# Kernel optimization log

Hardware: AMD Instinct MI355X
Metric: run time of the kernel (lower is better)

## Reference

```python
import jax, jax.numpy as jnp
import numpy as np

B, N, DX, DZ = 4, 2048, 2, 128
PPD = (128, 128)
GRID_RANGE = ((-2.0, 2.0), (-2.0, 2.0))
INIT_LS = 0.1


def _construct_grid():
    axes = [jnp.linspace(lo, hi, p, dtype=jnp.float32) for (lo, hi), p in zip(GRID_RANGE, PPD)]
    mesh = jnp.meshgrid(*axes, indexing="ij")
    return jnp.stack(mesh, axis=-1)  # [128, 128, 2]


def setup_inputs() -> dict:
    key = jax.random.key(0)
    k1, k2 = jax.random.split(key)
    x = jax.random.uniform(k1, (B, N, DX), dtype=jnp.float32, minval=-2.0, maxval=2.0)
    z = jax.random.normal(k2, (B, N, DZ), dtype=jnp.float32)
    grid = _construct_grid()
    # inverse-softplus of init lengthscale, per dim
    ls0 = jnp.full((DX,), INIT_LS, dtype=jnp.float32)
    lengthscale_param = jnp.log(jnp.exp(ls0) - 1.0)
    return {"x": x, "z": z, "grid": grid, "lengthscale_param": lengthscale_param}


def reference(x, z, grid, lengthscale_param):
    b = x.shape[0]
    grid_shape = grid.shape[:-1]  # (128, 128)
    lengthscale = 1e-05 + jax.nn.softplus(lengthscale_param)  # [dx]
    grid_flat = grid.reshape(-1, grid.shape[-1])  # [M, dx], M = 16384
    # per-dim squared distance / l^2, summed over dx  -> [b, M, n]
    diff = grid_flat[None, :, None, :] - x[:, None, :, :]  # [b, M, n, dx]
    pre_exp = jnp.sum((diff * diff) / (lengthscale ** 2), axis=-1)
    weights = jnp.exp(-0.5 * pre_exp)  # [b, M, n]
    z_grid_flat = jnp.einsum("bmn,bnd->bmd", weights, z)  # [b, M, dz]
    z_grid = z_grid_flat.reshape((b,) + grid_shape + (z.shape[-1],))
    x_grid = jnp.broadcast_to(grid[None], (b,) + grid.shape)
    return (x_grid, z_grid)
```

## Files before the change

### kernel.cpp

```cpp
#include <hip/hip_runtime.h>

#define BATCH 4
#define NPTS  2048
#define DZDIM 128
#define GD    128
#define M_TOT (GD*GD)
#define TN    32
#define PZ    40
#define ZP    2112
#define WBIN  15

typedef __attribute__((ext_vector_type(8))) __bf16 bf16x8;
typedef __attribute__((ext_vector_type(4))) float floatx4;

__device__ __forceinline__ unsigned int f2bf_bits(float x){
  unsigned int u = __float_as_uint(x);
  u += 0x7FFFu + ((u >> 16) & 1u);
  return u >> 16;
}
__device__ __forceinline__ int point_bin(float px){
  int bin = __float2int_rn((px + 2.0f) * (127.0f / 4.0f));
  return min(GD - 1, max(0, bin));
}

__global__ __launch_bounds__(256) void prep_kernel(
    const float* __restrict__ x, const float* __restrict__ grid,
    float* __restrict__ out, int* __restrict__ binStart,
    float2* __restrict__ xs, int* __restrict__ perm)
{
  const int tid = threadIdx.x;
  if (blockIdx.x < BATCH){
    __shared__ int h[GD];
    __shared__ int s[GD + 1];
    const int b = blockIdx.x;
    const float2* __restrict__ x2 = (const float2*)x;
    if (tid < GD) h[tid] = 0;
    __syncthreads();
    float2 xv[8]; int bn[8];
#pragma unroll
    for (int u = 0; u < 8; ++u){
      xv[u] = x2[b*NPTS + u*256 + tid];
      bn[u] = point_bin(xv[u].x);
      atomicAdd(&h[bn[u]], 1);
    }
    __syncthreads();
    if (tid == 0){
      int acc = 0;
#pragma unroll
      for (int j = 0; j < GD; ++j){ s[j] = acc; acc += h[j]; }
      s[GD] = acc;
    }
    __syncthreads();
    if (tid <= GD) binStart[b*(GD+1) + tid] = s[tid];
    if (tid < GD) h[tid] = 0;
    __syncthreads();
#pragma unroll
    for (int u = 0; u < 8; ++u){
      int j = s[bn[u]] + atomicAdd(&h[bn[u]], 1);
      xs[(long)b*ZP + j]       = xv[u];
      perm[b*NPTS + j]         = u*256 + tid;
    }
  } else {
    int idx = (blockIdx.x - BATCH) * 256 + tid;
    float g = grid[idx];
#pragma unroll
    for (int bb = 0; bb < BATCH; ++bb) out[bb*(GD*GD*2) + idx] = g;
  }
}

__global__ __launch_bounds__(256) void ztwy_kernel(
    const float* __restrict__ z, const float2* __restrict__ xs,
    const int* __restrict__ perm, const float* __restrict__ lsp,
    unsigned short* __restrict__ zt, float* __restrict__ wy)
{
  const int b   = blockIdx.y;
  const int jj  = threadIdx.x & 31;
  const int oct = threadIdx.x >> 5;
  if (blockIdx.x >= NPTS/32){
    int j = NPTS + (blockIdx.x - NPTS/32)*32 + jj;
#pragma unroll
    for (int yy = 0; yy < 16; ++yy)
      wy[(long)(b*GD + oct*16 + yy)*ZP + j] = 0.f;
    return;
  }
  const int j = blockIdx.x*32 + jj;
  const int n = perm[b*NPTS + j];
  const float4* __restrict__ z4 = (const float4*)z;
  const long rb = (long)(b*NPTS + n) * 32;
#pragma unroll
  for (int r = 0; r < 4; ++r){
    int c = oct*4 + r;
    float4 v = z4[rb + c];
    long o = ((long)(b*DZDIM + 4*c) * ZP) + j;
    zt[o        ] = (unsigned short)f2bf_bits(v.x);
    zt[o +   ZP ] = (unsigned short)f2bf_bits(v.y);
    zt[o + 2*ZP ] = (unsigned short)f2bf_bits(v.z);
    zt[o + 3*ZP ] = (unsigned short)f2bf_bits(v.w);
  }
  const float l1 = 1e-5f + log1pf(expf(lsp[1]));
  const float c1 = -0.5f * 1.4426950408889634f / (l1*l1);
  const float step = 4.0f / 127.0f;
  const float y = xs[(long)b*ZP + j].y;
  float gy = -2.0f + (float)(oct*16) * step;
#pragma unroll
  for (int yy = 0; yy < 16; ++yy){
    float d = gy - y;
    wy[(long)(b*GD + oct*16 + yy)*ZP + j] = __builtin_amdgcn_exp2f(c1*d*d);
    gy += step;
  }
}

__global__ __launch_bounds__(256, 4) void setconv_mfma_kernel(
    const float2* __restrict__ xs, const int* __restrict__ binStart,
    const unsigned short* __restrict__ zt, const float* __restrict__ wy,
    const float* __restrict__ lsp, float* __restrict__ outz)
{
  __shared__ __align__(16) unsigned short Zlds[2][DZDIM * PZ];
  __shared__ __align__(16) float Wx[2][TN];

  const int tid = threadIdx.x, lane = tid & 63, wv = tid >> 6;
  const int bid = blockIdx.x;
  const int g   = bid & 7;
  const int s   = bid >> 3;
  const int h   = s & 1;
  const int b   = (s >> 1) & 3;
  const int il  = s >> 3;
  const int i   = g*16 + il;
  const int my0 = h * 64;

  const float l0 = 1e-5f + log1pf(expf(lsp[0]));
  const float c0 = -0.5f * 1.4426950408889634f / (l0*l0);
  const float step = 4.0f / 127.0f;
  const float gx   = -2.0f + (float)i * step;

  const int lo  = binStart[b*(GD+1) + max(0, i - WBIN)];
  const int hi  = binStart[b*(GD+1) + min(GD-1, i + WBIN) + 1];
  const int lo8 = lo & ~7;
  const int len = hi - lo8;
  const int T   = (len + TN - 1) / TN;

  int goff[3];
#pragma unroll
  for (int u = 0; u < 3; ++u){
    int gi = wv + 4*u;
    if (gi < 10){
      int pos = gi*64 + lane;
      int d = pos / 5, c = pos % 5;
      if (c > 3) c = 3;
      goff[u] = (b*DZDIM + d) * ZP + c*8;
    } else goff[u] = 0;
  }

  const int q  = lane >> 4;
  const int ml = lane & 15;
  const float* __restrict__ wyp = wy + (long)(b*GD + my0 + wv*16 + ml) * ZP + q*8;

  floatx4 acc[8];
#pragma unroll
  for (int tz = 0; tz < 8; ++tz) acc[tz] = (floatx4){0.f, 0.f, 0.f, 0.f};

  auto stageZ = [&](int buf, int t){
    const int k0 = lo8 + t*TN;
#pragma unroll
    for (int u = 0; u < 3; ++u){
      int gi = wv + 4*u;
      if (gi < 10){
        const unsigned short* gp = zt + goff[u] + k0;
        __builtin_amdgcn_global_load_lds(
            (__attribute__((address_space(1))) void*)gp,
            (__attribute__((address_space(3))) void*)&Zlds[buf][gi*512],
            16, 0, 0);
      }
    }
  };
  auto stageWx = [&](int buf, int t){
    if (tid < TN){
      int ka = t*TN + tid;
      float2 xv = xs[(long)b*ZP + lo8 + ka];
      float d = gx - xv.x;
      float w = __builtin_amdgcn_exp2f(c0*d*d);
      Wx[buf][tid] = (ka < len) ? w : 0.f;
    }
  };

  if (T > 0){
    stageZ(0, 0);
    stageWx(0, 0);
    floatx4 wyA = *(const floatx4*)(wyp + lo8);
    floatx4 wyB = *(const floatx4*)(wyp + lo8 + 4);
    __syncthreads();
    for (int t = 0; t < T; ++t){
      const int cur = t & 1, nxt = 1 - cur;
      if (t + 1 < T){ stageZ(nxt, t + 1); stageWx(nxt, t + 1); }
      const int tp = (t + 1 < T) ? t + 1 : t;
      floatx4 nA = *(const floatx4*)(wyp + lo8 + tp*TN);
      floatx4 nB = *(const floatx4*)(wyp + lo8 + tp*TN + 4);
      floatx4 wx0 = *(const floatx4*)&Wx[cur][q*8];
      floatx4 wx1 = *(const floatx4*)&Wx[cur][q*8 + 4];
      float p0 = wyA[0]*wx0[0], p1 = wyA[1]*wx0[1], p2 = wyA[2]*wx0[2], p3 = wyA[3]*wx0[3];
      float p4 = wyB[0]*wx1[0], p5 = wyB[1]*wx1[1], p6 = wyB[2]*wx1[2], p7 = wyB[3]*wx1[3];
      union { unsigned int u[4]; bf16x8 v; } A;
      asm("v_cvt_pk_bf16_f32 %0, %1, %2" : "=v"(A.u[0]) : "v"(p0), "v"(p1));
      asm("v_cvt_pk_bf16_f32 %0, %1, %2" : "=v"(A.u[1]) : "v"(p2), "v"(p3));
      asm("v_cvt_pk_bf16_f32 %0, %1, %2" : "=v"(A.u[2]) : "v"(p4), "v"(p5));
      asm("v_cvt_pk_bf16_f32 %0, %1, %2" : "=v"(A.u[3]) : "v"(p6), "v"(p7));
      bf16x8 af = A.v;
#pragma unroll
      for (int tz = 0; tz < 8; ++tz){
        bf16x8 bf = *(const bf16x8*)&Zlds[cur][(tz*16 + ml)*PZ + q*8];
        acc[tz] = __builtin_amdgcn_mfma_f32_16x16x32_bf16(af, bf, acc[tz], 0, 0, 0);
      }
      __syncthreads();
      wyA = nA; wyB = nB;
    }
  }

  const long obase = ((long)(b*M_TOT + i*GD + my0 + wv*16 + q*4) << 7) + ml;
#pragma unroll
  for (int tz = 0; tz < 8; ++tz)
#pragma unroll
    for (int r = 0; r < 4; ++r)
      outz[obase + ((long)r << 7) + tz*16] = acc[tz][r];
}

extern "C" void kernel_launch(void* const* d_in, const int* in_sizes, int n_in,
                              void* d_out, int out_size, void* d_ws, size_t ws_size,
                              hipStream_t stream)
{
  const float* x    = (const float*)d_in[0];
  const float* z    = (const float*)d_in[1];
  const float* grid = (const float*)d_in[2];
  const float* lsp  = (const float*)d_in[3];
  float* out = (float*)d_out;

  char* ws = (char*)d_ws;
  int*            binStart = (int*)ws;
  int*            perm     = (int*)(ws + 2064);
  float2*         xs       = (float2*)(ws + 34832);
  unsigned short* zt       = (unsigned short*)(ws + 102416);
  float*          wy       = (float*)(ws + 2265104);

  hipLaunchKernelGGL(prep_kernel, dim3(BATCH + GD), dim3(256), 0, stream,
                     x, grid, out, binStart, xs, perm);
  hipLaunchKernelGGL(ztwy_kernel, dim3(NPTS/32 + 2, BATCH), dim3(256), 0, stream,
                     z, xs, perm, lsp, zt, wy);
  hipLaunchKernelGGL(setconv_mfma_kernel, dim3(GD*2*BATCH), dim3(256), 0, stream,
                     xs, binStart, zt, wy, lsp, out + BATCH*GD*GD*2);
}
```

Measured before the change: 108.0 us.

## Have each block compute both y-halves to reuse staged Z tiles

```diff
diff --git a/kernel.cpp b/kernel.cpp
--- a/kernel.cpp
+++ b/kernel.cpp
@@ -110,7 +110,7 @@
   }
 }
 
-__global__ __launch_bounds__(256, 4) void setconv_mfma_kernel(
+__global__ __launch_bounds__(256, 2) void setconv_mfma_kernel(
     const float2* __restrict__ xs, const int* __restrict__ binStart,
     const unsigned short* __restrict__ zt, const float* __restrict__ wy,
     const float* __restrict__ lsp, float* __restrict__ outz)
@@ -122,11 +122,9 @@
   const int bid = blockIdx.x;
   const int g   = bid & 7;
   const int s   = bid >> 3;
-  const int h   = s & 1;
-  const int b   = (s >> 1) & 3;
-  const int il  = s >> 3;
+  const int b   = s & 3;
+  const int il  = s >> 2;
   const int i   = g*16 + il;
-  const int my0 = h * 64;
 
   const float l0 = 1e-5f + log1pf(expf(lsp[0]));
   const float c0 = -0.5f * 1.4426950408889634f / (l0*l0);
@@ -153,11 +151,13 @@
 
   const int q  = lane >> 4;
   const int ml = lane & 15;
-  const float* __restrict__ wyp = wy + (long)(b*GD + my0 + wv*16 + ml) * ZP + q*8;
-
-  floatx4 acc[8];
-#pragma unroll
-  for (int tz = 0; tz < 8; ++tz) acc[tz] = (floatx4){0.f, 0.f, 0.f, 0.f};
+  const float* __restrict__ wyp = wy + (long)(b*GD + wv*16 + ml) * ZP + q*8;
+
+  floatx4 acc[2][8];
+#pragma unroll
+  for (int hh = 0; hh < 2; ++hh)
+#pragma unroll
+    for (int tz = 0; tz < 8; ++tz) acc[hh][tz] = (floatx4){0.f, 0.f, 0.f, 0.f};
 
   auto stageZ = [&](int buf, int t){
     const int k0 = lo8 + t*TN;
@@ -186,41 +186,59 @@
   if (T > 0){
     stageZ(0, 0);
     stageWx(0, 0);
-    floatx4 wyA = *(const floatx4*)(wyp + lo8);
-    floatx4 wyB = *(const floatx4*)(wyp + lo8 + 4);
+    floatx4 wA0 = *(const floatx4*)(wyp + lo8);
+    floatx4 wB0 = *(const floatx4*)(wyp + lo8 + 4);
+    floatx4 wA1 = *(const floatx4*)(wyp + 64*ZP + lo8);
+    floatx4 wB1 = *(const floatx4*)(wyp + 64*ZP + lo8 + 4);
     __syncthreads();
     for (int t = 0; t < T; ++t){
       const int cur = t & 1, nxt = 1 - cur;
       if (t + 1 < T){ stageZ(nxt, t + 1); stageWx(nxt, t + 1); }
       const int tp = (t + 1 < T) ? t + 1 : t;
-      floatx4 nA = *(const floatx4*)(wyp + lo8 + tp*TN);
-      floatx4 nB = *(const floatx4*)(wyp + lo8 + tp*TN + 4);
+      floatx4 nA0 = *(const floatx4*)(wyp + lo8 + tp*TN);
+      floatx4 nB0 = *(const floatx4*)(wyp + lo8 + tp*TN + 4);
+      floatx4 nA1 = *(const floatx4*)(wyp + 64*ZP + lo8 + tp*TN);
+      floatx4 nB1 = *(const floatx4*)(wyp + 64*ZP + lo8 + tp*TN + 4);
       floatx4 wx0 = *(const floatx4*)&Wx[cur][q*8];
       floatx4 wx1 = *(const floatx4*)&Wx[cur][q*8 + 4];
-      float p0 = wyA[0]*wx0[0], p1 = wyA[1]*wx0[1], p2 = wyA[2]*wx0[2], p3 = wyA[3]*wx0[3];
-      float p4 = wyB[0]*wx1[0], p5 = wyB[1]*wx1[1], p6 = wyB[2]*wx1[2], p7 = wyB[3]*wx1[3];
-      union { unsigned int u[4]; bf16x8 v; } A;
-      asm("v_cvt_pk_bf16_f32 %0, %1, %2" : "=v"(A.u[0]) : "v"(p0), "v"(p1));
-      asm("v_cvt_pk_bf16_f32 %0, %1, %2" : "=v"(A.u[1]) : "v"(p2), "v"(p3));
-      asm("v_cvt_pk_bf16_f32 %0, %1, %2" : "=v"(A.u[2]) : "v"(p4), "v"(p5));
-      asm("v_cvt_pk_bf16_f32 %0, %1, %2" : "=v"(A.u[3]) : "v"(p6), "v"(p7));
-      bf16x8 af = A.v;
+      union { unsigned int u[4]; bf16x8 v; } A0, A1;
+      {
+        float p0 = wA0[0]*wx0[0], p1 = wA0[1]*wx0[1], p2 = wA0[2]*wx0[2], p3 = wA0[3]*wx0[3];
+        float p4 = wB0[0]*wx1[0], p5 = wB0[1]*wx1[1], p6 = wB0[2]*wx1[2], p7 = wB0[3]*wx1[3];
+        asm("v_cvt_pk_bf16_f32 %0, %1, %2" : "=v"(A0.u[0]) : "v"(p0), "v"(p1));
+        asm("v_cvt_pk_bf16_f32 %0, %1, %2" : "=v"(A0.u[1]) : "v"(p2), "v"(p3));
+        asm("v_cvt_pk_bf16_f32 %0, %1, %2" : "=v"(A0.u[2]) : "v"(p4), "v"(p5));
+        asm("v_cvt_pk_bf16_f32 %0, %1, %2" : "=v"(A0.u[3]) : "v"(p6), "v"(p7));
+      }
+      {
+        float p0 = wA1[0]*wx0[0], p1 = wA1[1]*wx0[1], p2 = wA1[2]*wx0[2], p3 = wA1[3]*wx0[3];
+        float p4 = wB1[0]*wx1[0], p5 = wB1[1]*wx1[1], p6 = wB1[2]*wx1[2], p7 = wB1[3]*wx1[3];
+        asm("v_cvt_pk_bf16_f32 %0, %1, %2" : "=v"(A1.u[0]) : "v"(p0), "v"(p1));
+        asm("v_cvt_pk_bf16_f32 %0, %1, %2" : "=v"(A1.u[1]) : "v"(p2), "v"(p3));
+        asm("v_cvt_pk_bf16_f32 %0, %1, %2" : "=v"(A1.u[2]) : "v"(p4), "v"(p5));
+        asm("v_cvt_pk_bf16_f32 %0, %1, %2" : "=v"(A1.u[3]) : "v"(p6), "v"(p7));
+      }
+      bf16x8 af0 = A0.v, af1 = A1.v;
 #pragma unroll
       for (int tz = 0; tz < 8; ++tz){
         bf16x8 bf = *(const bf16x8*)&Zlds[cur][(tz*16 + ml)*PZ + q*8];
-        acc[tz] = __builtin_amdgcn_mfma_f32_16x16x32_bf16(af, bf, acc[tz], 0, 0, 0);
+        acc[0][tz] = __builtin_amdgcn_mfma_f32_16x16x32_bf16(af0, bf, acc[0][tz], 0, 0, 0);
+        acc[1][tz] = __builtin_amdgcn_mfma_f32_16x16x32_bf16(af1, bf, acc[1][tz], 0, 0, 0);
       }
       __syncthreads();
-      wyA = nA; wyB = nB;
-    }
-  }
-
-  const long obase = ((long)(b*M_TOT + i*GD + my0 + wv*16 + q*4) << 7) + ml;
-#pragma unroll
-  for (int tz = 0; tz < 8; ++tz)
-#pragma unroll
-    for (int r = 0; r < 4; ++r)
-      outz[obase + ((long)r << 7) + tz*16] = acc[tz][r];
+      wA0 = nA0; wB0 = nB0; wA1 = nA1; wB1 = nB1;
+    }
+  }
+
+#pragma unroll
+  for (int hh = 0; hh < 2; ++hh){
+    const long obase = ((long)(b*M_TOT + i*GD + hh*64 + wv*16 + q*4) << 7) + ml;
+#pragma unroll
+    for (int tz = 0; tz < 8; ++tz)
+#pragma unroll
+      for (int r = 0; r < 4; ++r)
+        outz[obase + ((long)r << 7) + tz*16] = acc[hh][tz][r];
+  }
 }
 
 extern "C" void kernel_launch(void* const* d_in, const int* in_sizes, int n_in,
@@ -244,6 +262,6 @@
                      x, grid, out, binStart, xs, perm);
   hipLaunchKernelGGL(ztwy_kernel, dim3(NPTS/32 + 2, BATCH), dim3(256), 0, stream,
                      z, xs, perm, lsp, zt, wy);
-  hipLaunchKernelGGL(setconv_mfma_kernel, dim3(GD*2*BATCH), dim3(256), 0, stream,
+  hipLaunchKernelGGL(setconv_mfma_kernel, dim3(GD*BATCH), dim3(256), 0, stream,
                      xs, binStart, zt, wy, lsp, out + BATCH*GD*GD*2);
 }
```

Result: no change. 106.6 us (-1.4%).
